# Optimization experiments

Hardware: AMD Instinct MI355X
Metric: run time of the kernel (lower is better)

The kernel has to match this reference:

```python
import jax, jax.numpy as jnp
import numpy as np

D_MODEL = 768
NUM_HEADS = 12
DEPTH = D_MODEL // NUM_HEADS


def setup_inputs() -> dict:
    key = jax.random.key(0)
    ks = jax.random.split(key, 11)
    B, S, D = 2, 2048, D_MODEL
    scale = 1.0 / np.sqrt(D)
    inp = {
        "v": jax.random.normal(ks[0], (B, S, D), jnp.float32),
        "k": jax.random.normal(ks[1], (B, S, D), jnp.float32),
        "q": jax.random.normal(ks[2], (B, S, D), jnp.float32),
        "wq": jax.random.normal(ks[3], (D, D), jnp.float32) * scale,
        "bq": jnp.zeros((D,), jnp.float32),
        "wk": jax.random.normal(ks[4], (D, D), jnp.float32) * scale,
        "bk": jnp.zeros((D,), jnp.float32),
        "wv": jax.random.normal(ks[5], (D, D), jnp.float32) * scale,
        "bv": jnp.zeros((D,), jnp.float32),
        "wo": jax.random.normal(ks[6], (D, D), jnp.float32) * scale,
        "bo": jnp.zeros((D,), jnp.float32),
    }
    return inp


def _split_heads(x):
    # (B, S, D) -> (B, H, S, depth)
    B, S, _ = x.shape
    return x.reshape(B, S, NUM_HEADS, DEPTH).transpose(0, 2, 1, 3)


def reference(v, k, q, wq, bq, wk, bk, wv, bv, wo, bo):
    B, S, D = q.shape
    qh = _split_heads(q @ wq + bq)  # (B,H,S,dh)
    kh = _split_heads(k @ wk + bk)
    vh = _split_heads(v @ wv + bv)
    logits = jnp.einsum("bhqd,bhkd->bhqk", qh, kh) / jnp.sqrt(
        jnp.asarray(DEPTH, qh.dtype)
    )
    attn = jax.nn.softmax(logits, axis=-1)  # (B,H,S,S)
    ctx = jnp.einsum("bhqk,bhkd->bhqd", attn, vh)
    ctx = ctx.transpose(0, 2, 1, 3).reshape(B, S, D)
    return ctx @ wo + bo
```

## Files before the change

### kernel.cpp

```cpp
#include <hip/hip_runtime.h>
#include <hip/hip_bf16.h>
#include <math.h>

typedef __bf16 bf16;
typedef __attribute__((ext_vector_type(8))) __bf16 bf16x8;
typedef __attribute__((ext_vector_type(4))) __bf16 bf16x4v;
typedef __attribute__((ext_vector_type(4))) float f32x4;

#define MFMA16(a, b, c) __builtin_amdgcn_mfma_f32_16x16x32_bf16(a, b, c, 0, 0, 0)

__device__ __forceinline__ void gld16(const bf16* g, bf16* l) {
  __builtin_amdgcn_global_load_lds((const __attribute__((address_space(1))) void*)g,
                                   (__attribute__((address_space(3))) void*)l, 16, 0, 0);
}

__global__ __launch_bounds__(256) void prep(const float* __restrict__ q,
                                            const float* __restrict__ k,
                                            const float* __restrict__ v,
                                            bf16* __restrict__ qb, bf16* __restrict__ kb,
                                            bf16* __restrict__ vb,
                                            const float* __restrict__ w0,
                                            const float* __restrict__ w1,
                                            const float* __restrict__ w2,
                                            const float* __restrict__ w3,
                                            bf16* __restrict__ t0, bf16* __restrict__ t1,
                                            bf16* __restrict__ t2, bf16* __restrict__ t3) {
  const int lin = blockIdx.x;
  if (lin < 4608) {
    const int which = lin / 1536, idx = lin % 1536;
    const float* a = which == 0 ? q : (which == 1 ? k : v);
    bf16* o = which == 0 ? qb : (which == 1 ? kb : vb);
    const size_t i = ((size_t)idx * 256 + threadIdx.x) * 8;
    const float4 f0 = *(const float4*)(a + i);
    const float4 f1 = *(const float4*)(a + i + 4);
    bf16x8 r = {(bf16)f0.x, (bf16)f0.y, (bf16)f0.z, (bf16)f0.w,
                (bf16)f1.x, (bf16)f1.y, (bf16)f1.z, (bf16)f1.w};
    *(bf16x8*)(o + i) = r;
  } else {
    const int w = lin - 4608;
    const int z = w / 576, rem = w % 576;
    const int by = rem / 24, bx = rem % 24;
    const float* W = z == 0 ? w0 : (z == 1 ? w1 : (z == 2 ? w2 : w3));
    bf16* T = z == 0 ? t0 : (z == 1 ? t1 : (z == 2 ? t2 : t3));
    __shared__ float t[32][33];
    const int tx = threadIdx.x & 31, ty = threadIdx.x >> 5;
    const int c0 = bx * 32, r0 = by * 32;
#pragma unroll
    for (int i = 0; i < 4; ++i) {
      const int r = ty + 8 * i;
      t[r][tx] = W[(size_t)(r0 + r) * 768 + c0 + tx];
    }
    __syncthreads();
#pragma unroll
    for (int i = 0; i < 4; ++i) {
      const int r = ty + 8 * i;
      T[(size_t)(c0 + r) * 768 + r0 + tx] = (bf16)t[tx][r];
    }
  }
}

__device__ __forceinline__ void gemm_core(const bf16* __restrict__ A, const bf16* __restrict__ BT,
                                          int row0, int col0, bf16* As, bf16* Bs,
                                          f32x4 acc[4][4]) {
  const int tid = threadIdx.x;
  const int lane = tid & 63, wave = tid >> 6;
  const int m15 = lane & 15, kg = lane >> 4;
  const int wm = wave >> 1, wn = wave & 1;
  const int pr16 = lane & 15;
  const int pk8 = (lane >> 4) * 8;
#pragma unroll
  for (int i = 0; i < 4; ++i)
#pragma unroll
    for (int j = 0; j < 4; ++j) acc[i][j] = f32x4{0.f, 0.f, 0.f, 0.f};

  for (int k0 = 0; k0 < 768; k0 += 32) {
#pragma unroll
    for (int j = 0; j < 2; ++j) {
      const int i = wave * 2 + j;
      gld16(A + (size_t)(row0 + 16 * i + pr16) * 768 + k0 + pk8, As + i * 512);
      gld16(BT + (size_t)(col0 + 16 * i + pr16) * 768 + k0 + pk8, Bs + i * 512);
    }
    __syncthreads();
    bf16x8 af[4], bfr[4];
#pragma unroll
    for (int t = 0; t < 4; ++t)
      af[t] = *(const bf16x8*)(As + (4 * wm + t) * 512 + kg * 128 + m15 * 8);
#pragma unroll
    for (int t = 0; t < 4; ++t)
      bfr[t] = *(const bf16x8*)(Bs + (4 * wn + t) * 512 + kg * 128 + m15 * 8);
#pragma unroll
    for (int mt = 0; mt < 4; ++mt)
#pragma unroll
      for (int nt = 0; nt < 4; ++nt) acc[mt][nt] = MFMA16(af[mt], bfr[nt], acc[mt][nt]);
    __syncthreads();
  }
}

__global__ __launch_bounds__(256, 3) void gemm_qkv(
    const bf16* __restrict__ qb, const bf16* __restrict__ kb, const bf16* __restrict__ vb,
    const bf16* __restrict__ wqT, const bf16* __restrict__ wkT, const bf16* __restrict__ wvT,
    const float* __restrict__ bq, const float* __restrict__ bk, const float* __restrict__ bv,
    bf16* __restrict__ Qh, bf16* __restrict__ Kh, bf16* __restrict__ Vt) {
  __shared__ bf16 As[128 * 32], Bs[128 * 32];
  const bf16 *A, *BT;
  const float* bias;
  bf16* out;
  int mode;
  if (blockIdx.z == 0) { A = qb; BT = wqT; bias = bq; out = Qh; mode = 0; }
  else if (blockIdx.z == 1) { A = kb; BT = wkT; bias = bk; out = Kh; mode = 0; }
  else { A = vb; BT = wvT; bias = bv; out = Vt; mode = 1; }
  const int row0 = blockIdx.y * 128, col0 = blockIdx.x * 128;
  f32x4 acc[4][4];
  gemm_core(A, BT, row0, col0, As, Bs, acc);

  const int lane = threadIdx.x & 63, wave = threadIdx.x >> 6;
  const int m15 = lane & 15, kg = lane >> 4;
  const int wm = wave >> 1, wn = wave & 1;
#pragma unroll
  for (int mt = 0; mt < 4; ++mt) {
#pragma unroll
    for (int nt = 0; nt < 4; ++nt) {
      const int col = col0 + 64 * wn + 16 * nt + m15;
      const float bb = bias[col];
      const int h = col >> 6, d = col & 63;
      const int rowb = row0 + 64 * wm + 16 * mt + kg * 4;
      const int b = rowb >> 11, s0 = rowb & 2047;
      if (mode == 0) {
#pragma unroll
        for (int r = 0; r < 4; ++r)
          out[((size_t)(b * 12 + h) * 2048 + s0 + r) * 64 + d] = (bf16)(acc[mt][nt][r] + bb);
      } else {
        bf16x4v pk;
#pragma unroll
        for (int r = 0; r < 4; ++r) pk[r] = (bf16)(acc[mt][nt][r] + bb);
        *(bf16x4v*)&out[((size_t)(b * 12 + h) * 64 + d) * 2048 + s0] = pk;
      }
    }
  }
}

__global__ __launch_bounds__(256, 3) void gemm_out(const bf16* __restrict__ A,
                                                   const bf16* __restrict__ BT,
                                                   const float* __restrict__ bias,
                                                   float* __restrict__ out) {
  __shared__ bf16 As[64 * 32], Bs[64 * 32];
  const int tid = threadIdx.x;
  const int lane = tid & 63, wave = tid >> 6;
  const int m15 = lane & 15, kg = lane >> 4;
  const int wm = wave >> 1, wn = wave & 1;
  const int row0 = blockIdx.y * 64, col0 = blockIdx.x * 64;
  const int kh = blockIdx.z;
  const int pr16 = lane & 15, pk8 = (lane >> 4) * 8;

  f32x4 acc[2][2];
#pragma unroll
  for (int i = 0; i < 2; ++i)
#pragma unroll
    for (int j = 0; j < 2; ++j) acc[i][j] = f32x4{0.f, 0.f, 0.f, 0.f};

  for (int k0 = kh * 384; k0 < kh * 384 + 384; k0 += 32) {
    gld16(A + (size_t)(row0 + 16 * wave + pr16) * 768 + k0 + pk8, As + wave * 512);
    gld16(BT + (size_t)(col0 + 16 * wave + pr16) * 768 + k0 + pk8, Bs + wave * 512);
    __syncthreads();
    bf16x8 af[2], bfr[2];
#pragma unroll
    for (int t = 0; t < 2; ++t)
      af[t] = *(const bf16x8*)(As + (2 * wm + t) * 512 + kg * 128 + m15 * 8);
#pragma unroll
    for (int t = 0; t < 2; ++t)
      bfr[t] = *(const bf16x8*)(Bs + (2 * wn + t) * 512 + kg * 128 + m15 * 8);
#pragma unroll
    for (int mt = 0; mt < 2; ++mt)
#pragma unroll
      for (int nt = 0; nt < 2; ++nt) acc[mt][nt] = MFMA16(af[mt], bfr[nt], acc[mt][nt]);
    __syncthreads();
  }
#pragma unroll
  for (int mt = 0; mt < 2; ++mt) {
#pragma unroll
    for (int nt = 0; nt < 2; ++nt) {
      const int col = col0 + 32 * wn + 16 * nt + m15;
      const float bb = (kh == 0) ? bias[col] : 0.f;
#pragma unroll
      for (int r = 0; r < 4; ++r) {
        const int row = row0 + 32 * wm + 16 * mt + kg * 4 + r;
        atomicAdd(&out[(size_t)row * 768 + col], acc[mt][nt][r] + bb);
      }
    }
  }
}

__global__ __launch_bounds__(128, 2) void attn_kernel(const bf16* __restrict__ Q,
                                                      const bf16* __restrict__ K,
                                                      const bf16* __restrict__ VT,
                                                      bf16* __restrict__ ctx) {
  __shared__ __align__(16) char SMEM[20480];

  const int tid = threadIdx.x;
  const int lane = tid & 63, wave = tid >> 6;
  const int m15 = lane & 15, kg = lane >> 4;
  const int lin = blockIdx.x;
  const int bh = lin % 24, rg = lin / 24;
  const size_t hb = (size_t)bh * 2048 * 64;
  const bf16* Qp = Q + hb;
  const bf16* Kp = K + hb;
  const bf16* Vp = VT + hb;
  const int qrow0 = rg * 64;
  bf16* Pw = (bf16*)SMEM + wave * 2048;

  bf16x8 qf[4][2];
#pragma unroll
  for (int t = 0; t < 4; ++t)
#pragma unroll
    for (int ks = 0; ks < 2; ++ks) {
      bf16x8 tv = *(const bf16x8*)&Qp[(size_t)(qrow0 + 16 * t + m15) * 64 + 32 * ks + kg * 8];
#pragma unroll
      for (int j = 0; j < 8; ++j) tv[j] = (bf16)((float)tv[j] * 0.125f);
      qf[t][ks] = tv;
    }

  f32x4 o[4][4];
  float lp[4][4];
#pragma unroll
  for (int t = 0; t < 4; ++t) {
#pragma unroll
    for (int nt = 0; nt < 4; ++nt) o[t][nt] = f32x4{0.f, 0.f, 0.f, 0.f};
#pragma unroll
    for (int r = 0; r < 4; ++r) lp[t][r] = 0.f;
  }

  const int kbase = wave * 1024;
  for (int c = 0; c < 32; ++c) {
    const int kc = kbase + c * 32;
    bf16x8 kf[2][2];
#pragma unroll
    for (int nt = 0; nt < 2; ++nt)
#pragma unroll
      for (int ks = 0; ks < 2; ++ks)
        kf[nt][ks] = *(const bf16x8*)&Kp[(size_t)(kc + 16 * nt + m15) * 64 + 32 * ks + kg * 8];
    bf16x8 vf[4];
#pragma unroll
    for (int nt = 0; nt < 4; ++nt)
      vf[nt] = *(const bf16x8*)&Vp[(size_t)(16 * nt + m15) * 2048 + kc + kg * 8];
    f32x4 s[4][2];
#pragma unroll
    for (int t = 0; t < 4; ++t)
#pragma unroll
      for (int nt = 0; nt < 2; ++nt) s[t][nt] = f32x4{0.f, 0.f, 0.f, 0.f};
#pragma unroll
    for (int ks = 0; ks < 2; ++ks)
#pragma unroll
      for (int nt = 0; nt < 2; ++nt)
#pragma unroll
        for (int t = 0; t < 4; ++t) s[t][nt] = MFMA16(qf[t][ks], kf[nt][ks], s[t][nt]);
#pragma unroll
    for (int t = 0; t < 4; ++t)
#pragma unroll
      for (int r = 0; r < 4; ++r)
#pragma unroll
        for (int nt = 0; nt < 2; ++nt) {
          const float pe = __expf(s[t][nt][r]);
          lp[t][r] += pe;
          const int col = 16 * nt + m15;
          Pw[t * 512 + (col >> 3) * 128 + (kg * 4 + r) * 8 + (col & 7)] = (bf16)pe;
        }
    asm volatile("s_waitcnt lgkmcnt(0)" ::: "memory");
#pragma unroll
    for (int t = 0; t < 4; ++t) {
      const bf16x8 pf = *(const bf16x8*)&Pw[t * 512 + kg * 128 + m15 * 8];
#pragma unroll
      for (int nt = 0; nt < 4; ++nt) o[t][nt] = MFMA16(pf, vf[nt], o[t][nt]);
    }
  }

  __syncthreads();
  float* sc = (float*)SMEM;
  if (wave == 1) {
#pragma unroll
    for (int t = 0; t < 4; ++t) {
#pragma unroll
      for (int nt = 0; nt < 4; ++nt)
        *(f32x4*)&sc[((t * 4 + nt) * 64 + lane) * 4] = o[t][nt];
      f32x4 l = {lp[t][0], lp[t][1], lp[t][2], lp[t][3]};
      *(f32x4*)&sc[4096 + (t * 64 + lane) * 4] = l;
    }
  }
  __syncthreads();
  if (wave == 0) {
#pragma unroll
    for (int t = 0; t < 4; ++t) {
#pragma unroll
      for (int nt = 0; nt < 4; ++nt) {
        const f32x4 po = *(const f32x4*)&sc[((t * 4 + nt) * 64 + lane) * 4];
#pragma unroll
        for (int j = 0; j < 4; ++j) o[t][nt][j] += po[j];
      }
      const f32x4 pl = *(const f32x4*)&sc[4096 + (t * 64 + lane) * 4];
#pragma unroll
      for (int r = 0; r < 4; ++r) lp[t][r] += pl[r];
    }
#pragma unroll
    for (int t = 0; t < 4; ++t)
#pragma unroll
      for (int r = 0; r < 4; ++r) {
#pragma unroll
        for (int st = 1; st < 16; st <<= 1) lp[t][r] += __shfl_xor(lp[t][r], st);
      }
    const int b = bh / 12, h = bh % 12;
#pragma unroll
    for (int t = 0; t < 4; ++t)
#pragma unroll
      for (int nt = 0; nt < 4; ++nt)
#pragma unroll
        for (int r = 0; r < 4; ++r) {
          const int sr = qrow0 + 16 * t + kg * 4 + r;
          ctx[((size_t)(b * 2048) + sr) * 768 + h * 64 + 16 * nt + m15] =
              (bf16)(o[t][nt][r] / lp[t][r]);
        }
  }
}

extern "C" void kernel_launch(void* const* d_in, const int* in_sizes, int n_in,
                              void* d_out, int out_size, void* d_ws, size_t ws_size,
                              hipStream_t stream) {
  const float* v = (const float*)d_in[0];
  const float* k = (const float*)d_in[1];
  const float* q = (const float*)d_in[2];
  const float* wq = (const float*)d_in[3];
  const float* bq = (const float*)d_in[4];
  const float* wk = (const float*)d_in[5];
  const float* bk = (const float*)d_in[6];
  const float* wv = (const float*)d_in[7];
  const float* bv = (const float*)d_in[8];
  const float* wo = (const float*)d_in[9];
  const float* bo = (const float*)d_in[10];

  char* ws = (char*)d_ws;
  const size_t SEG = (size_t)4096 * 768 * sizeof(bf16);
  const size_t WSEG = (size_t)768 * 768 * sizeof(bf16);
  bf16* Qh = (bf16*)(ws + 0 * SEG);
  bf16* Kh = (bf16*)(ws + 1 * SEG);
  bf16* Vt = (bf16*)(ws + 2 * SEG);
  bf16* qb = (bf16*)(ws + 3 * SEG);
  bf16* kb = (bf16*)(ws + 4 * SEG);
  bf16* vb = (bf16*)(ws + 5 * SEG);
  bf16* ctx = qb;
  bf16* wqT = (bf16*)(ws + 6 * SEG);
  bf16* wkT = (bf16*)(ws + 6 * SEG + WSEG);
  bf16* wvT = (bf16*)(ws + 6 * SEG + 2 * WSEG);
  bf16* woT = (bf16*)(ws + 6 * SEG + 3 * WSEG);

  hipMemsetAsync(d_out, 0, (size_t)out_size * sizeof(float), stream);

  prep<<<dim3(6912), 256, 0, stream>>>(q, k, v, qb, kb, vb, wq, wk, wv, wo,
                                       wqT, wkT, wvT, woT);
  gemm_qkv<<<dim3(6, 32, 3), 256, 0, stream>>>(qb, kb, vb, wqT, wkT, wvT, bq, bk, bv,
                                               Qh, Kh, Vt);
  attn_kernel<<<dim3(768), 128, 0, stream>>>(Qh, Kh, Vt, ctx);
  gemm_out<<<dim3(12, 64, 2), 256, 0, stream>>>(ctx, woT, bo, (float*)d_out);
}
```

Before: 232.6 us.

## Split attention keys across four waves, transpose score MFMA, drop split-K atomics

The attention kernel now runs 4 waves per block, each handling a quarter of the keys instead of half. Scores are computed transposed (K×Q) so P can be packed as 4-element vector stores into a padded LDS tile, and partial outputs are combined through a two-step LDS tree reduction. The output GEMM drops its split-K atomics and the memset for a single full-K pass with plain stores. The extra waves add parallelism and latency hiding, at the cost of more LDS, an extra reduction step, and fewer output-GEMM blocks.

```diff
diff --git a/kernel.cpp b/kernel.cpp
--- a/kernel.cpp
+++ b/kernel.cpp
@@ -149,7 +149,6 @@
   const int m15 = lane & 15, kg = lane >> 4;
   const int wm = wave >> 1, wn = wave & 1;
   const int row0 = blockIdx.y * 64, col0 = blockIdx.x * 64;
-  const int kh = blockIdx.z;
   const int pr16 = lane & 15, pk8 = (lane >> 4) * 8;
 
   f32x4 acc[2][2];
@@ -158,7 +157,7 @@
 #pragma unroll
     for (int j = 0; j < 2; ++j) acc[i][j] = f32x4{0.f, 0.f, 0.f, 0.f};
 
-  for (int k0 = kh * 384; k0 < kh * 384 + 384; k0 += 32) {
+  for (int k0 = 0; k0 < 768; k0 += 32) {
     gld16(A + (size_t)(row0 + 16 * wave + pr16) * 768 + k0 + pk8, As + wave * 512);
     gld16(BT + (size_t)(col0 + 16 * wave + pr16) * 768 + k0 + pk8, Bs + wave * 512);
     __syncthreads();
@@ -180,21 +179,21 @@
 #pragma unroll
     for (int nt = 0; nt < 2; ++nt) {
       const int col = col0 + 32 * wn + 16 * nt + m15;
-      const float bb = (kh == 0) ? bias[col] : 0.f;
+      const float bb = bias[col];
 #pragma unroll
       for (int r = 0; r < 4; ++r) {
         const int row = row0 + 32 * wm + 16 * mt + kg * 4 + r;
-        atomicAdd(&out[(size_t)row * 768 + col], acc[mt][nt][r] + bb);
-      }
-    }
-  }
-}
-
-__global__ __launch_bounds__(128, 2) void attn_kernel(const bf16* __restrict__ Q,
+        out[(size_t)row * 768 + col] = acc[mt][nt][r] + bb;
+      }
+    }
+  }
+}
+
+__global__ __launch_bounds__(256, 3) void attn_kernel(const bf16* __restrict__ Q,
                                                       const bf16* __restrict__ K,
                                                       const bf16* __restrict__ VT,
                                                       bf16* __restrict__ ctx) {
-  __shared__ __align__(16) char SMEM[20480];
+  __shared__ __align__(16) char SMEM[33792];
 
   const int tid = threadIdx.x;
   const int lane = tid & 63, wave = tid >> 6;
@@ -206,117 +205,134 @@
   const bf16* Kp = K + hb;
   const bf16* Vp = VT + hb;
   const int qrow0 = rg * 64;
-  bf16* Pw = (bf16*)SMEM + wave * 2048;
+  bf16* Pw = (bf16*)SMEM + wave * 2560;
 
   bf16x8 qf[4][2];
 #pragma unroll
-  for (int t = 0; t < 4; ++t)
+  for (int rt = 0; rt < 4; ++rt)
 #pragma unroll
     for (int ks = 0; ks < 2; ++ks) {
-      bf16x8 tv = *(const bf16x8*)&Qp[(size_t)(qrow0 + 16 * t + m15) * 64 + 32 * ks + kg * 8];
+      bf16x8 tv = *(const bf16x8*)&Qp[(size_t)(qrow0 + 16 * rt + m15) * 64 + 32 * ks + kg * 8];
 #pragma unroll
       for (int j = 0; j < 8; ++j) tv[j] = (bf16)((float)tv[j] * 0.125f);
-      qf[t][ks] = tv;
+      qf[rt][ks] = tv;
     }
 
   f32x4 o[4][4];
-  float lp[4][4];
-#pragma unroll
-  for (int t = 0; t < 4; ++t) {
-#pragma unroll
-    for (int nt = 0; nt < 4; ++nt) o[t][nt] = f32x4{0.f, 0.f, 0.f, 0.f};
-#pragma unroll
-    for (int r = 0; r < 4; ++r) lp[t][r] = 0.f;
-  }
-
-  const int kbase = wave * 1024;
-  for (int c = 0; c < 32; ++c) {
+  float lp[4];
+#pragma unroll
+  for (int rt = 0; rt < 4; ++rt) {
+#pragma unroll
+    for (int mt = 0; mt < 4; ++mt) o[rt][mt] = f32x4{0.f, 0.f, 0.f, 0.f};
+    lp[rt] = 0.f;
+  }
+
+  const int kbase = wave * 512;
+  for (int c = 0; c < 16; ++c) {
     const int kc = kbase + c * 32;
     bf16x8 kf[2][2];
 #pragma unroll
-    for (int nt = 0; nt < 2; ++nt)
+    for (int kt = 0; kt < 2; ++kt)
 #pragma unroll
       for (int ks = 0; ks < 2; ++ks)
-        kf[nt][ks] = *(const bf16x8*)&Kp[(size_t)(kc + 16 * nt + m15) * 64 + 32 * ks + kg * 8];
+        kf[kt][ks] = *(const bf16x8*)&Kp[(size_t)(kc + 16 * kt + m15) * 64 + 32 * ks + kg * 8];
     bf16x8 vf[4];
 #pragma unroll
-    for (int nt = 0; nt < 4; ++nt)
-      vf[nt] = *(const bf16x8*)&Vp[(size_t)(16 * nt + m15) * 2048 + kc + kg * 8];
-    f32x4 s[4][2];
-#pragma unroll
-    for (int t = 0; t < 4; ++t)
-#pragma unroll
-      for (int nt = 0; nt < 2; ++nt) s[t][nt] = f32x4{0.f, 0.f, 0.f, 0.f};
+    for (int mt = 0; mt < 4; ++mt)
+      vf[mt] = *(const bf16x8*)&Vp[(size_t)(16 * mt + m15) * 2048 + kc + kg * 8];
+    f32x4 s[2][4];
+#pragma unroll
+    for (int kt = 0; kt < 2; ++kt)
+#pragma unroll
+      for (int rt = 0; rt < 4; ++rt) s[kt][rt] = f32x4{0.f, 0.f, 0.f, 0.f};
 #pragma unroll
     for (int ks = 0; ks < 2; ++ks)
 #pragma unroll
-      for (int nt = 0; nt < 2; ++nt)
-#pragma unroll
-        for (int t = 0; t < 4; ++t) s[t][nt] = MFMA16(qf[t][ks], kf[nt][ks], s[t][nt]);
-#pragma unroll
-    for (int t = 0; t < 4; ++t)
-#pragma unroll
-      for (int r = 0; r < 4; ++r)
-#pragma unroll
-        for (int nt = 0; nt < 2; ++nt) {
-          const float pe = __expf(s[t][nt][r]);
-          lp[t][r] += pe;
-          const int col = 16 * nt + m15;
-          Pw[t * 512 + (col >> 3) * 128 + (kg * 4 + r) * 8 + (col & 7)] = (bf16)pe;
+      for (int kt = 0; kt < 2; ++kt)
+#pragma unroll
+        for (int rt = 0; rt < 4; ++rt) s[kt][rt] = MFMA16(kf[kt][ks], qf[rt][ks], s[kt][rt]);
+#pragma unroll
+    for (int kt = 0; kt < 2; ++kt)
+#pragma unroll
+      for (int rt = 0; rt < 4; ++rt) {
+        bf16x4v pk;
+#pragma unroll
+        for (int r = 0; r < 4; ++r) {
+          const float pe = __expf(s[kt][rt][r]);
+          lp[rt] += pe;
+          pk[r] = (bf16)pe;
         }
+        *(bf16x4v*)&Pw[rt * 640 + m15 * 40 + 16 * kt + 4 * kg] = pk;
+      }
     asm volatile("s_waitcnt lgkmcnt(0)" ::: "memory");
 #pragma unroll
-    for (int t = 0; t < 4; ++t) {
-      const bf16x8 pf = *(const bf16x8*)&Pw[t * 512 + kg * 128 + m15 * 8];
-#pragma unroll
-      for (int nt = 0; nt < 4; ++nt) o[t][nt] = MFMA16(pf, vf[nt], o[t][nt]);
-    }
-  }
-
+    for (int rt = 0; rt < 4; ++rt) {
+      const bf16x8 pf = *(const bf16x8*)&Pw[rt * 640 + m15 * 40 + kg * 8];
+#pragma unroll
+      for (int mt = 0; mt < 4; ++mt) o[rt][mt] = MFMA16(vf[mt], pf, o[rt][mt]);
+    }
+  }
+
+#pragma unroll
+  for (int rt = 0; rt < 4; ++rt) {
+    lp[rt] += __shfl_xor(lp[rt], 16);
+    lp[rt] += __shfl_xor(lp[rt], 32);
+  }
+
+  float* R0 = (float*)SMEM;
+  float* R1 = (float*)(SMEM + 16384);
+  float* LP = (float*)(SMEM + 32768);
   __syncthreads();
-  float* sc = (float*)SMEM;
-  if (wave == 1) {
-#pragma unroll
-    for (int t = 0; t < 4; ++t) {
-#pragma unroll
-      for (int nt = 0; nt < 4; ++nt)
-        *(f32x4*)&sc[((t * 4 + nt) * 64 + lane) * 4] = o[t][nt];
-      f32x4 l = {lp[t][0], lp[t][1], lp[t][2], lp[t][3]};
-      *(f32x4*)&sc[4096 + (t * 64 + lane) * 4] = l;
-    }
+  if (kg == 0) {
+#pragma unroll
+    for (int rt = 0; rt < 4; ++rt) LP[wave * 64 + rt * 16 + m15] = lp[rt];
+  }
+  if (wave == 1 || wave == 3) {
+    float* R = (wave == 1) ? R0 : R1;
+#pragma unroll
+    for (int rt = 0; rt < 4; ++rt)
+#pragma unroll
+      for (int mt = 0; mt < 4; ++mt)
+        *(f32x4*)&R[((rt * 4 + mt) * 64 + lane) * 4] = o[rt][mt];
+  }
+  __syncthreads();
+  if (wave == 0 || wave == 2) {
+    float* R = (wave == 0) ? R0 : R1;
+#pragma unroll
+    for (int rt = 0; rt < 4; ++rt)
+#pragma unroll
+      for (int mt = 0; mt < 4; ++mt) {
+        const f32x4 po = *(const f32x4*)&R[((rt * 4 + mt) * 64 + lane) * 4];
+#pragma unroll
+        for (int j = 0; j < 4; ++j) o[rt][mt][j] += po[j];
+      }
+  }
+  __syncthreads();
+  if (wave == 2) {
+#pragma unroll
+    for (int rt = 0; rt < 4; ++rt)
+#pragma unroll
+      for (int mt = 0; mt < 4; ++mt)
+        *(f32x4*)&R1[((rt * 4 + mt) * 64 + lane) * 4] = o[rt][mt];
   }
   __syncthreads();
   if (wave == 0) {
-#pragma unroll
-    for (int t = 0; t < 4; ++t) {
-#pragma unroll
-      for (int nt = 0; nt < 4; ++nt) {
-        const f32x4 po = *(const f32x4*)&sc[((t * 4 + nt) * 64 + lane) * 4];
-#pragma unroll
-        for (int j = 0; j < 4; ++j) o[t][nt][j] += po[j];
-      }
-      const f32x4 pl = *(const f32x4*)&sc[4096 + (t * 64 + lane) * 4];
-#pragma unroll
-      for (int r = 0; r < 4; ++r) lp[t][r] += pl[r];
-    }
-#pragma unroll
-    for (int t = 0; t < 4; ++t)
-#pragma unroll
-      for (int r = 0; r < 4; ++r) {
-#pragma unroll
-        for (int st = 1; st < 16; st <<= 1) lp[t][r] += __shfl_xor(lp[t][r], st);
-      }
     const int b = bh / 12, h = bh % 12;
 #pragma unroll
-    for (int t = 0; t < 4; ++t)
-#pragma unroll
-      for (int nt = 0; nt < 4; ++nt)
-#pragma unroll
-        for (int r = 0; r < 4; ++r) {
-          const int sr = qrow0 + 16 * t + kg * 4 + r;
-          ctx[((size_t)(b * 2048) + sr) * 768 + h * 64 + 16 * nt + m15] =
-              (bf16)(o[t][nt][r] / lp[t][r]);
-        }
+    for (int rt = 0; rt < 4; ++rt) {
+      const float lsum = LP[0 * 64 + rt * 16 + m15] + LP[1 * 64 + rt * 16 + m15] +
+                         LP[2 * 64 + rt * 16 + m15] + LP[3 * 64 + rt * 16 + m15];
+      const float inv = 1.0f / lsum;
+      const int sr = qrow0 + 16 * rt + m15;
+#pragma unroll
+      for (int mt = 0; mt < 4; ++mt) {
+        const f32x4 po = *(const f32x4*)&R1[((rt * 4 + mt) * 64 + lane) * 4];
+        bf16x4v pk;
+#pragma unroll
+        for (int r = 0; r < 4; ++r) pk[r] = (bf16)((o[rt][mt][r] + po[r]) * inv);
+        *(bf16x4v*)&ctx[((size_t)(b * 2048) + sr) * 768 + h * 64 + 16 * mt + 4 * kg] = pk;
+      }
+    }
   }
 }
 
@@ -350,12 +366,10 @@
   bf16* wvT = (bf16*)(ws + 6 * SEG + 2 * WSEG);
   bf16* woT = (bf16*)(ws + 6 * SEG + 3 * WSEG);
 
-  hipMemsetAsync(d_out, 0, (size_t)out_size * sizeof(float), stream);
-
   prep<<<dim3(6912), 256, 0, stream>>>(q, k, v, qb, kb, vb, wq, wk, wv, wo,
                                        wqT, wkT, wvT, woT);
   gemm_qkv<<<dim3(6, 32, 3), 256, 0, stream>>>(qb, kb, vb, wqT, wkT, wvT, bq, bk, bv,
                                                Qh, Kh, Vt);
-  attn_kernel<<<dim3(768), 128, 0, stream>>>(Qh, Kh, Vt, ctx);
-  gemm_out<<<dim3(12, 64, 2), 256, 0, stream>>>(ctx, woT, bo, (float*)d_out);
-}
+  attn_kernel<<<dim3(768), 256, 0, stream>>>(Qh, Kh, Vt, ctx);
+  gemm_out<<<dim3(12, 64), 256, 0, stream>>>(ctx, woT, bo, (float*)d_out);
+}
```

New measurement: 217.9 us. 1.07x faster.
